# Kernel optimization log

Hardware: AMD Instinct MI355X
Metric: run time of the kernel (lower is better)

The kernel has to match this reference:

```python
import jax, jax.numpy as jnp
import numpy as np

B, T, C, H = 4, 4096, 1024, 64

def setup_inputs() -> dict:
    key = jax.random.key(0)
    k1, k2, k3, k4, k5 = jax.random.split(key, 5)
    scale = 0.02
    return {
        "x": jax.random.normal(k1, (B, T, C), dtype=jnp.float32),
        "head_bias": jax.random.normal(k2, (T, T), dtype=jnp.float32) * 0.1,
        "w_k": jax.random.normal(k3, (C, H), dtype=jnp.float32) * scale,
        "w_q": jax.random.normal(k4, (C, H), dtype=jnp.float32) * scale,
        "w_v": jax.random.normal(k5, (C, H), dtype=jnp.float32) * scale,
    }

def reference(x, head_bias, w_k, w_q, w_v):
    # x: (B,T,C) ; projections: (B,T,H)
    k = jnp.einsum('btc,ch->bth', x, w_k)
    q = jnp.einsum('btc,ch->bth', x, w_q)
    v = jnp.einsum('btc,ch->bth', x, w_v)
    Tq = x.shape[1]
    # scores: (B,T,T) with RPE bias and causal mask
    scores = jnp.einsum('bqh,bkh->bqk', q, k) * (k.shape[-1] ** -0.5)
    scores = scores + head_bias[None, :, :]
    causal = jnp.tril(jnp.ones((Tq, Tq), dtype=bool))
    scores = jnp.where(causal[None, :, :], scores, -jnp.inf)
    weights = jax.nn.softmax(scores, axis=-1)
    out = jnp.einsum('bqk,bkh->bqh', weights, v)
    return out
```

## Files before the change

kernel.cpp:

```cpp
#include <hip/hip_runtime.h>
#include <hip/hip_bf16.h>


#define T_DIM 4096
#define C_DIM 1024
#define CK    256

typedef __attribute__((ext_vector_type(8))) short s16x8;
typedef __attribute__((ext_vector_type(4))) float f32x4;
typedef __attribute__((ext_vector_type(2))) unsigned int u32x2;

__device__ __forceinline__ short f2bf(float f) {
    unsigned u = __builtin_bit_cast(unsigned, f);
    u += 0x7FFFu + ((u >> 16) & 1u);
    return (short)(u >> 16);
}
__device__ __forceinline__ unsigned pack2(float a, float b) {
    unsigned ua = __builtin_bit_cast(unsigned, a);
    unsigned ub = __builtin_bit_cast(unsigned, b);
    ua += 0x7FFFu + ((ua >> 16) & 1u);
    ub += 0x7FFFu + ((ub >> 16) & 1u);
    return __builtin_amdgcn_perm(ub, ua, 0x07060302u);
}
__device__ __forceinline__ float bf2f(short s) {
    unsigned u = ((unsigned)(unsigned short)s) << 16;
    return __builtin_bit_cast(float, u);
}
__device__ __forceinline__ int chunk_off(int qt) {
    int g = qt >> 4, r = qt & 15;
    return qt + 8 * g * (g - 1) + r * g;
}
__device__ __forceinline__ void async16(const short* g, short* l) {
    __builtin_amdgcn_global_load_lds(
        (const __attribute__((address_space(1))) unsigned int*)g,
        (__attribute__((address_space(3))) unsigned int*)l, 16, 0, 0);
}

__global__ __launch_bounds__(256) void prep_frag(
    const float* __restrict__ wk, const float* __restrict__ wq,
    const float* __restrict__ wv, short* __restrict__ wfrag)
{
    int ksAll = blockIdx.x, mat = blockIdx.y;
    const float* w = (mat == 0) ? wk : ((mat == 1) ? wq : wv);
    float sc = (mat == 1) ? 0.125f : 1.0f;
    int nt = threadIdx.x >> 6, lane = threadIdx.x & 63;
    int quad = lane >> 4, l15 = lane & 15;
    int h = nt * 16 + l15;
    int cb = ksAll * 32 + quad * 8;
    s16x8 v;
    #pragma unroll
    for (int j = 0; j < 8; ++j) v[j] = f2bf(w[(cb + j) * 64 + h] * sc);
    *(s16x8*)&wfrag[((ksAll * 12 + mat * 4 + nt) * 64 + lane) * 8] = v;
}

union ProjSmem {
    short xs[32][1032];
    struct {
        short comb[2][16][136];
        short vsep[64][40];
    } c;
};

__global__ __launch_bounds__(256, 2) void proj_fused(
    const float* __restrict__ x, const short* __restrict__ wfrag,
    short* __restrict__ qb, short* __restrict__ kfrag, short* __restrict__ vfrag)
{
    __shared__ __align__(16) ProjSmem sm;

    int tid = threadIdx.x;
    int w = tid >> 6, lane = tid & 63;
    int rt = w >> 1, h = w & 1;
    int l15 = lane & 15, quad = lane >> 4;
    int m0 = blockIdx.x * 32;

    s16x8 fA[12], fB[12];
    {
        const s16x8* fb = (const s16x8*)&wfrag[((size_t)(h * 16) * 12 * 64 + lane) * 8];
        #pragma unroll
        for (int f = 0; f < 12; ++f) fA[f] = fb[f * 64];
    }

    #pragma unroll 8
    for (int p = 0; p < 32; ++p) {
        f32x4 v = *(const f32x4*)&x[(size_t)(m0 + p) * C_DIM + tid * 4];
        u32x2 d;
        d[0] = pack2(v[0], v[1]);
        d[1] = pack2(v[2], v[3]);
        *(u32x2*)&sm.xs[p][tid * 4] = d;
    }
    __syncthreads();

    f32x4 acc[12];
    #pragma unroll
    for (int i = 0; i < 12; ++i) acc[i] = (f32x4){0.f, 0.f, 0.f, 0.f};

    #pragma unroll 1
    for (int ks = 0; ks < 16; ks += 2) {
        {
            const s16x8* fb = (const s16x8*)&wfrag[((size_t)(h * 16 + ks + 1) * 12 * 64 + lane) * 8];
            #pragma unroll
            for (int f = 0; f < 12; ++f) fB[f] = fb[f * 64];
        }
        s16x8 af = *(const s16x8*)&sm.xs[rt * 16 + l15][(h * 16 + ks) * 32 + quad * 8];
        #pragma unroll
        for (int f = 0; f < 12; ++f)
            acc[f] = __builtin_amdgcn_mfma_f32_16x16x32_bf16(af, fA[f], acc[f], 0, 0, 0);
        if (ks + 2 < 16) {
            const s16x8* fb = (const s16x8*)&wfrag[((size_t)(h * 16 + ks + 2) * 12 * 64 + lane) * 8];
            #pragma unroll
            for (int f = 0; f < 12; ++f) fA[f] = fb[f * 64];
        }
        s16x8 af2 = *(const s16x8*)&sm.xs[rt * 16 + l15][(h * 16 + ks + 1) * 32 + quad * 8];
        #pragma unroll
        for (int f = 0; f < 12; ++f)
            acc[f] = __builtin_amdgcn_mfma_f32_16x16x32_bf16(af2, fB[f], acc[f], 0, 0, 0);
    }
    __syncthreads();

    if (h == 1) {
        #pragma unroll
        for (int f = 0; f < 8; ++f)
            #pragma unroll
            for (int r = 0; r < 4; ++r)
                sm.c.comb[rt][quad * 4 + r][(f >> 2) * 64 + (f & 3) * 16 + l15] = f2bf(acc[f][r]);
        #pragma unroll
        for (int f = 8; f < 12; ++f)
            #pragma unroll
            for (int r = 0; r < 4; ++r)
                sm.c.vsep[(f & 3) * 16 + l15][rt * 16 + quad * 4 + r] = f2bf(acc[f][r]);
    }
    __syncthreads();
    if (h == 0) {
        #pragma unroll
        for (int f = 0; f < 8; ++f)
            #pragma unroll
            for (int r = 0; r < 4; ++r) {
                int col = (f >> 2) * 64 + (f & 3) * 16 + l15, rr = quad * 4 + r;
                sm.c.comb[rt][rr][col] = f2bf(acc[f][r] + bf2f(sm.c.comb[rt][rr][col]));
            }
        #pragma unroll
        for (int f = 8; f < 12; ++f)
            #pragma unroll
            for (int r = 0; r < 4; ++r) {
                int hh = (f & 3) * 16 + l15, kk = rt * 16 + quad * 4 + r;
                sm.c.vsep[hh][kk] = f2bf(acc[f][r] + bf2f(sm.c.vsep[hh][kk]));
            }
    }
    __syncthreads();

    int b = m0 >> 12, t0 = m0 & 4095;
    int t016 = t0 >> 4, kt32 = t0 >> 5;
    {
        int row = tid >> 3, ch = tid & 7;
        s16x8 v = *(const s16x8*)&sm.c.comb[row >> 4][row & 15][64 + ch * 8];
        *(s16x8*)&qb[(size_t)(m0 + row) * 64 + ch * 8] = v;
    }
    {
        int kt = w & 1, ks = w >> 1;
        s16x8 v = *(const s16x8*)&sm.c.comb[kt][l15][ks * 32 + quad * 8];
        *(s16x8*)&kfrag[(size_t)(((b * 256 + t016 + kt) * 2 + ks) * 64 + lane) * 8] = v;
    }
    {
        int nt = w;
        s16x8 v = *(const s16x8*)&sm.c.vsep[nt * 16 + l15][quad * 8];
        *(s16x8*)&vfrag[(size_t)(((b * 128 + kt32) * 4 + nt) * 64 + lane) * 8] = v;
    }
}

#define SOFT(N, AS, BV) do {                                                  \
    float _sv[4];                                                             \
    _Pragma("unroll")                                                         \
    for (int _r = 0; _r < 4; ++_r) {                                          \
        _sv[_r] = (AS)[_r] + (BV)[_r];                                        \
        if (mask_on && (kabs + (N) * 16 + quad * 4 + _r > q0 + l15))          \
            _sv[_r] = -__builtin_inff();                                      \
        float _p = __expf(_sv[_r]);                                           \
        _sv[_r] = _p;                                                         \
        l_sum += _p;                                                          \
    }                                                                         \
    u32x2 _d;                                                                 \
    _d[0] = pack2(_sv[0], _sv[1]);                                            \
    _d[1] = pack2(_sv[2], _sv[3]);                                            \
    *(u32x2*)&plds[w][l15][(N) * 16 + quad * 4] = _d;                         \
} while (0)

#define COMPUTEK(KREL, B0, B1) do {                                           \
    int _kt16 = (KREL) >> 4;                                                  \
    int _kt32 = (KREL) >> 5;                                                  \
    int kabs = kstart + (KREL);                                               \
    s16x8 _ak0 = *(const s16x8*)&klds[(_kt16 * 2 + 0) * 512 + lane * 8];      \
    s16x8 _ak1 = *(const s16x8*)&klds[(_kt16 * 2 + 1) * 512 + lane * 8];      \
    s16x8 _ak2 = *(const s16x8*)&klds[(_kt16 * 2 + 2) * 512 + lane * 8];      \
    s16x8 _ak3 = *(const s16x8*)&klds[(_kt16 * 2 + 3) * 512 + lane * 8];      \
    s16x8 _bv0 = *(const s16x8*)&vlds[(_kt32 * 4 + 0) * 512 + lane * 8];      \
    s16x8 _bv1 = *(const s16x8*)&vlds[(_kt32 * 4 + 1) * 512 + lane * 8];      \
    s16x8 _bv2 = *(const s16x8*)&vlds[(_kt32 * 4 + 2) * 512 + lane * 8];      \
    s16x8 _bv3 = *(const s16x8*)&vlds[(_kt32 * 4 + 3) * 512 + lane * 8];      \
    f32x4 _aS0 = (f32x4){0.f, 0.f, 0.f, 0.f};                                 \
    f32x4 _aS1 = (f32x4){0.f, 0.f, 0.f, 0.f};                                 \
    _aS0 = __builtin_amdgcn_mfma_f32_16x16x32_bf16(_ak0, aq0, _aS0, 0, 0, 0); \
    _aS0 = __builtin_amdgcn_mfma_f32_16x16x32_bf16(_ak1, aq1, _aS0, 0, 0, 0); \
    _aS1 = __builtin_amdgcn_mfma_f32_16x16x32_bf16(_ak2, aq0, _aS1, 0, 0, 0); \
    _aS1 = __builtin_amdgcn_mfma_f32_16x16x32_bf16(_ak3, aq1, _aS1, 0, 0, 0); \
    SOFT(0, _aS0, B0);                                                        \
    SOFT(1, _aS1, B1);                                                        \
    s16x8 _ap = *(const s16x8*)&plds[w][l15][quad * 8];                       \
    accO[0] = __builtin_amdgcn_mfma_f32_16x16x32_bf16(_ap, _bv0, accO[0], 0, 0, 0); \
    accO[1] = __builtin_amdgcn_mfma_f32_16x16x32_bf16(_ap, _bv1, accO[1], 0, 0, 0); \
    accO[2] = __builtin_amdgcn_mfma_f32_16x16x32_bf16(_ap, _bv2, accO[2], 0, 0, 0); \
    accO[3] = __builtin_amdgcn_mfma_f32_16x16x32_bf16(_ap, _bv3, accO[3], 0, 0, 0); \
} while (0)

__global__ __launch_bounds__(512, 4) void flash_part(
    const short* __restrict__ qb, const short* __restrict__ kfrag,
    const short* __restrict__ vfrag, const float* __restrict__ bias,
    short* __restrict__ po)
{
    int g = blockIdx.x;
    int c = blockIdx.y;
    int b = blockIdx.z;
    if (c > (g >> 1)) return;

    __shared__ __align__(16) short klds[32 * 512];
    __shared__ __align__(16) short vlds[32 * 512];
    __shared__ __align__(16) short plds[8][16][40];

    int tid = threadIdx.x;
    int w = tid >> 6, lane = tid & 63;
    int l15 = lane & 15, quad = lane >> 4;

    int qt = g * 8 + w;
    int q0 = qt * 16;
    int kstart = c * CK;
    int kend = min(kstart + CK, q0 + 16);
    int nk = kend - kstart;
    bool mask_on = (kend > q0);

    const short* ksrc = kfrag + (size_t)((b * 256 + c * 16) * 2) * 512;
    const short* vsrc = vfrag + (size_t)((b * 128 + c * 8) * 4) * 512;
    #pragma unroll
    for (int i = 0; i < 4; ++i) {
        int seg = i * 8 + w;
        async16(ksrc + (size_t)seg * 512 + lane * 8, &klds[seg * 512]);
    }
    #pragma unroll
    for (int i = 0; i < 4; ++i) {
        int seg = i * 8 + w;
        async16(vsrc + (size_t)seg * 512 + lane * 8, &vlds[seg * 512]);
    }

    const short* qrow = qb + (size_t)(b * T_DIM + q0 + l15) * 64;
    s16x8 aq0 = *(const s16x8*)(qrow + quad * 8);
    s16x8 aq1 = *(const s16x8*)(qrow + 32 + quad * 8);
    const float* brow = bias + (size_t)(q0 + l15) * T_DIM + kstart;
    f32x4 bA0 = *(const f32x4*)&brow[quad * 4];
    f32x4 bA1 = *(const f32x4*)&brow[16 + quad * 4];
    f32x4 bB0, bB1;

    float l_sum = 0.f;
    f32x4 accO[4];
    #pragma unroll
    for (int nt = 0; nt < 4; ++nt) accO[nt] = (f32x4){0.f, 0.f, 0.f, 0.f};

    __syncthreads();

    int krel = 0;
    while (true) {
        int kn = krel + 32;
        bool more = (kn < nk);
        if (more) {
            bB0 = *(const f32x4*)&brow[kn + quad * 4];
            bB1 = *(const f32x4*)&brow[kn + 16 + quad * 4];
        }
        COMPUTEK(krel, bA0, bA1);
        if (!more) break;
        krel = kn; kn = krel + 32;
        bool more2 = (kn < nk);
        if (more2) {
            bA0 = *(const f32x4*)&brow[kn + quad * 4];
            bA1 = *(const f32x4*)&brow[kn + 16 + quad * 4];
        }
        COMPUTEK(krel, bB0, bB1);
        if (!more2) break;
        krel = kn;
    }

    l_sum += __shfl_xor(l_sum, 16, 64);
    l_sum += __shfl_xor(l_sum, 32, 64);

    short* base = po + (size_t)((chunk_off(qt) + c) * 4 + b) * 1040;
    #pragma unroll
    for (int nt = 0; nt < 4; ++nt)
        #pragma unroll
        for (int r = 0; r < 4; ++r)
            base[(quad * 4 + r) * 64 + nt * 16 + l15] = f2bf(accO[nt][r]);
    if (quad == 0) base[1024 + l15] = f2bf(l_sum);
}

__global__ __launch_bounds__(256) void flash_reduce(
    const short* __restrict__ po, float* __restrict__ out)
{
    int idx = blockIdx.x * 256 + threadIdx.x;
    int row = idx >> 3, c8 = idx & 7;
    int b = row >> 12, t = row & 4095;
    int qt = t >> 4, rloc = t & 15;
    int nc = (t >> 8) + 1;
    int off = chunk_off(qt);
    float o[8];
    #pragma unroll
    for (int j = 0; j < 8; ++j) o[j] = 0.f;
    float l = 0.f;
    #pragma unroll 1
    for (int cc = 0; cc < nc; ++cc) {
        const short* base = po + (size_t)((off + cc) * 4 + b) * 1040;
        s16x8 v = *(const s16x8*)&base[rloc * 64 + c8 * 8];
        #pragma unroll
        for (int j = 0; j < 8; ++j) o[j] += bf2f(v[j]);
        l += bf2f(base[1024 + rloc]);
    }
    float inv = 1.0f / l;
    f32x4 r0 = (f32x4){o[0] * inv, o[1] * inv, o[2] * inv, o[3] * inv};
    f32x4 r1 = (f32x4){o[4] * inv, o[5] * inv, o[6] * inv, o[7] * inv};
    float* op = &out[(size_t)row * 64 + c8 * 8];
    *(f32x4*)op = r0;
    *(f32x4*)(op + 4) = r1;
}

extern "C" void kernel_launch(void* const* d_in, const int* in_sizes, int n_in,
                              void* d_out, int out_size, void* d_ws, size_t ws_size,
                              hipStream_t stream) {
    (void)in_sizes; (void)n_in; (void)out_size; (void)ws_size;
    const float* x    = (const float*)d_in[0];
    const float* bias = (const float*)d_in[1];
    const float* wk   = (const float*)d_in[2];
    const float* wq   = (const float*)d_in[3];
    const float* wv   = (const float*)d_in[4];
    float* out = (float*)d_out;

    short* wfrag = (short*)d_ws;
    short* qb    = wfrag + 196608;
    short* kfrag = qb + 1048576;
    short* vfrag = kfrag + 1048576;
    short* po    = vfrag + 1048576;

    prep_frag<<<dim3(32, 3), dim3(256), 0, stream>>>(wk, wq, wv, wfrag);
    proj_fused<<<dim3(512), dim3(256), 0, stream>>>(x, wfrag, qb, kfrag, vfrag);
    flash_part<<<dim3(32, 16, 4), dim3(512), 0, stream>>>(qb, kfrag, vfrag, bias, po);
    flash_reduce<<<dim3(512), dim3(256), 0, stream>>>(po, out);
}
```

Baseline: 204.5 us.

## Double-buffer K/V staging in 64-key slices and shuffle P via permlane swaps

Replaces the single upfront load of the full 256-key K/V chunk into LDS with double-buffered 64-key slices, so the async copy of the next slice overlaps compute on the current one. Bias prefetch moves to 64-key granularity. The probability tile no longer round-trips through LDS; it is rearranged into MFMA A-operand layout with v_permlane32/16_swap instructions. LDS drops substantially and the occupancy hint rises from 4 to 6, at the cost of a __syncthreads per slice and extra register pressure.

After: 234.3 us. +14.6%, slower.

```diff
diff --git a/kernel.cpp b/kernel.cpp
--- a/kernel.cpp
+++ b/kernel.cpp
@@ -5,10 +5,12 @@
 #define T_DIM 4096
 #define C_DIM 1024
 #define CK    256
+#define SK    64
 
 typedef __attribute__((ext_vector_type(8))) short s16x8;
 typedef __attribute__((ext_vector_type(4))) float f32x4;
 typedef __attribute__((ext_vector_type(2))) unsigned int u32x2;
+typedef __attribute__((ext_vector_type(4))) unsigned int u32x4;
 
 __device__ __forceinline__ short f2bf(float f) {
     unsigned u = __builtin_bit_cast(unsigned, f);
@@ -167,7 +169,19 @@
     }
 }
 
-#define SOFT(N, AS, BV) do {                                                  \
+#define STAGE(S, KB, VB) do {                                                 \
+    async16(ksrc + (size_t)((S) * 8 + w) * 512 + lane * 8, &KB[w * 512]);     \
+    async16(vsrc + (size_t)((S) * 8 + w) * 512 + lane * 8, &VB[w * 512]);     \
+} while (0)
+
+#define BIAS4(KREL, D0, D1, D2, D3) do {                                      \
+    D0 = *(const f32x4*)&brow[(KREL) + quad * 4];                             \
+    D1 = *(const f32x4*)&brow[(KREL) + 16 + quad * 4];                        \
+    D2 = *(const f32x4*)&brow[(KREL) + 32 + quad * 4];                        \
+    D3 = *(const f32x4*)&brow[(KREL) + 48 + quad * 4];                        \
+} while (0)
+
+#define SOFT(N, AS, BV, PLO, PHI) do {                                        \
     float _sv[4];                                                             \
     _Pragma("unroll")                                                         \
     for (int _r = 0; _r < 4; ++_r) {                                          \
@@ -178,40 +192,44 @@
         _sv[_r] = _p;                                                         \
         l_sum += _p;                                                          \
     }                                                                         \
-    u32x2 _d;                                                                 \
-    _d[0] = pack2(_sv[0], _sv[1]);                                            \
-    _d[1] = pack2(_sv[2], _sv[3]);                                            \
-    *(u32x2*)&plds[w][l15][(N) * 16 + quad * 4] = _d;                         \
+    PLO = pack2(_sv[0], _sv[1]);                                              \
+    PHI = pack2(_sv[2], _sv[3]);                                              \
 } while (0)
 
-#define COMPUTEK(KREL, B0, B1) do {                                           \
-    int _kt16 = (KREL) >> 4;                                                  \
-    int _kt32 = (KREL) >> 5;                                                  \
+#define COMPUTEK(KB, VB, KREL, B0, B1) do {                                   \
+    int _lt = (((KREL) & 63) >> 4);                               \
+    int _lv = (((KREL) & 63) >> 5);                               \
     int kabs = kstart + (KREL);                                               \
-    s16x8 _ak0 = *(const s16x8*)&klds[(_kt16 * 2 + 0) * 512 + lane * 8];      \
-    s16x8 _ak1 = *(const s16x8*)&klds[(_kt16 * 2 + 1) * 512 + lane * 8];      \
-    s16x8 _ak2 = *(const s16x8*)&klds[(_kt16 * 2 + 2) * 512 + lane * 8];      \
-    s16x8 _ak3 = *(const s16x8*)&klds[(_kt16 * 2 + 3) * 512 + lane * 8];      \
-    s16x8 _bv0 = *(const s16x8*)&vlds[(_kt32 * 4 + 0) * 512 + lane * 8];      \
-    s16x8 _bv1 = *(const s16x8*)&vlds[(_kt32 * 4 + 1) * 512 + lane * 8];      \
-    s16x8 _bv2 = *(const s16x8*)&vlds[(_kt32 * 4 + 2) * 512 + lane * 8];      \
-    s16x8 _bv3 = *(const s16x8*)&vlds[(_kt32 * 4 + 3) * 512 + lane * 8];      \
+    s16x8 _ak0 = *(const s16x8*)&KB[(_lt * 2 + 0) * 512 + lane * 8];          \
+    s16x8 _ak1 = *(const s16x8*)&KB[(_lt * 2 + 1) * 512 + lane * 8];          \
+    s16x8 _ak2 = *(const s16x8*)&KB[(_lt * 2 + 2) * 512 + lane * 8];          \
+    s16x8 _ak3 = *(const s16x8*)&KB[(_lt * 2 + 3) * 512 + lane * 8];          \
     f32x4 _aS0 = (f32x4){0.f, 0.f, 0.f, 0.f};                                 \
     f32x4 _aS1 = (f32x4){0.f, 0.f, 0.f, 0.f};                                 \
     _aS0 = __builtin_amdgcn_mfma_f32_16x16x32_bf16(_ak0, aq0, _aS0, 0, 0, 0); \
     _aS0 = __builtin_amdgcn_mfma_f32_16x16x32_bf16(_ak1, aq1, _aS0, 0, 0, 0); \
     _aS1 = __builtin_amdgcn_mfma_f32_16x16x32_bf16(_ak2, aq0, _aS1, 0, 0, 0); \
     _aS1 = __builtin_amdgcn_mfma_f32_16x16x32_bf16(_ak3, aq1, _aS1, 0, 0, 0); \
-    SOFT(0, _aS0, B0);                                                        \
-    SOFT(1, _aS1, B1);                                                        \
-    s16x8 _ap = *(const s16x8*)&plds[w][l15][quad * 8];                       \
+    unsigned _p0, _p1, _p2, _p3;                                              \
+    SOFT(0, _aS0, B0, _p0, _p1);                                              \
+    SOFT(1, _aS1, B1, _p2, _p3);                                              \
+    asm("v_permlane32_swap_b32 %0, %1" : "+v"(_p0), "+v"(_p2));               \
+    asm("v_permlane16_swap_b32 %0, %1" : "+v"(_p0), "+v"(_p2));               \
+    asm("v_permlane32_swap_b32 %0, %1" : "+v"(_p1), "+v"(_p3));               \
+    asm("v_permlane16_swap_b32 %0, %1" : "+v"(_p1), "+v"(_p3));               \
+    u32x4 _apu = (u32x4){_p0, _p1, _p2, _p3};                                 \
+    s16x8 _ap = __builtin_bit_cast(s16x8, _apu);                              \
+    s16x8 _bv0 = *(const s16x8*)&VB[(_lv * 4 + 0) * 512 + lane * 8];          \
+    s16x8 _bv1 = *(const s16x8*)&VB[(_lv * 4 + 1) * 512 + lane * 8];          \
+    s16x8 _bv2 = *(const s16x8*)&VB[(_lv * 4 + 2) * 512 + lane * 8];          \
+    s16x8 _bv3 = *(const s16x8*)&VB[(_lv * 4 + 3) * 512 + lane * 8];          \
     accO[0] = __builtin_amdgcn_mfma_f32_16x16x32_bf16(_ap, _bv0, accO[0], 0, 0, 0); \
     accO[1] = __builtin_amdgcn_mfma_f32_16x16x32_bf16(_ap, _bv1, accO[1], 0, 0, 0); \
     accO[2] = __builtin_amdgcn_mfma_f32_16x16x32_bf16(_ap, _bv2, accO[2], 0, 0, 0); \
     accO[3] = __builtin_amdgcn_mfma_f32_16x16x32_bf16(_ap, _bv3, accO[3], 0, 0, 0); \
 } while (0)
 
-__global__ __launch_bounds__(512, 4) void flash_part(
+__global__ __launch_bounds__(512, 6) void flash_part(
     const short* __restrict__ qb, const short* __restrict__ kfrag,
     const short* __restrict__ vfrag, const float* __restrict__ bias,
     short* __restrict__ po)
@@ -221,9 +239,10 @@
     int b = blockIdx.z;
     if (c > (g >> 1)) return;
 
-    __shared__ __align__(16) short klds[32 * 512];
-    __shared__ __align__(16) short vlds[32 * 512];
-    __shared__ __align__(16) short plds[8][16][40];
+    __shared__ __align__(16) short klds0[8 * 512];
+    __shared__ __align__(16) short klds1[8 * 512];
+    __shared__ __align__(16) short vlds0[8 * 512];
+    __shared__ __align__(16) short vlds1[8 * 512];
 
     int tid = threadIdx.x;
     int w = tid >> 6, lane = tid & 63;
@@ -234,28 +253,20 @@
     int kstart = c * CK;
     int kend = min(kstart + CK, q0 + 16);
     int nk = kend - kstart;
+    int nkb = min(CK, 128 * g + 128 - kstart);
+    int nsub = (nkb + SK - 1) / SK;
     bool mask_on = (kend > q0);
 
     const short* ksrc = kfrag + (size_t)((b * 256 + c * 16) * 2) * 512;
     const short* vsrc = vfrag + (size_t)((b * 128 + c * 8) * 4) * 512;
-    #pragma unroll
-    for (int i = 0; i < 4; ++i) {
-        int seg = i * 8 + w;
-        async16(ksrc + (size_t)seg * 512 + lane * 8, &klds[seg * 512]);
-    }
-    #pragma unroll
-    for (int i = 0; i < 4; ++i) {
-        int seg = i * 8 + w;
-        async16(vsrc + (size_t)seg * 512 + lane * 8, &vlds[seg * 512]);
-    }
-
+
+    STAGE(0, klds0, vlds0);
     const short* qrow = qb + (size_t)(b * T_DIM + q0 + l15) * 64;
     s16x8 aq0 = *(const s16x8*)(qrow + quad * 8);
     s16x8 aq1 = *(const s16x8*)(qrow + 32 + quad * 8);
     const float* brow = bias + (size_t)(q0 + l15) * T_DIM + kstart;
-    f32x4 bA0 = *(const f32x4*)&brow[quad * 4];
-    f32x4 bA1 = *(const f32x4*)&brow[16 + quad * 4];
-    f32x4 bB0, bB1;
+    f32x4 bA0, bA1, bA2, bA3, bB0, bB1, bB2, bB3;
+    BIAS4(0, bA0, bA1, bA2, bA3);
 
     float l_sum = 0.f;
     f32x4 accO[4];
@@ -264,25 +275,24 @@
 
     __syncthreads();
 
-    int krel = 0;
+    int s = 0, krel = 0;
     while (true) {
-        int kn = krel + 32;
-        bool more = (kn < nk);
-        if (more) {
-            bB0 = *(const f32x4*)&brow[kn + quad * 4];
-            bB1 = *(const f32x4*)&brow[kn + 16 + quad * 4];
-        }
-        COMPUTEK(krel, bA0, bA1);
-        if (!more) break;
-        krel = kn; kn = krel + 32;
-        bool more2 = (kn < nk);
-        if (more2) {
-            bA0 = *(const f32x4*)&brow[kn + quad * 4];
-            bA1 = *(const f32x4*)&brow[kn + 16 + quad * 4];
-        }
-        COMPUTEK(krel, bB0, bB1);
-        if (!more2) break;
-        krel = kn;
+        bool hn = (s + 1 < nsub);
+        if (hn) STAGE(s + 1, klds1, vlds1);
+        if (krel < nk)      COMPUTEK(klds0, vlds0, krel, bA0, bA1);
+        if (krel + 32 < nk) COMPUTEK(klds0, vlds0, krel + 32, bA2, bA3);
+        if (hn) BIAS4(krel + 64, bB0, bB1, bB2, bB3);
+        __syncthreads();
+        if (!hn) break;
+        ++s; krel += SK;
+        bool hn2 = (s + 1 < nsub);
+        if (hn2) STAGE(s + 1, klds0, vlds0);
+        if (krel < nk)      COMPUTEK(klds1, vlds1, krel, bB0, bB1);
+        if (krel + 32 < nk) COMPUTEK(klds1, vlds1, krel + 32, bB2, bB3);
+        if (hn2) BIAS4(krel + 64, bA0, bA1, bA2, bA3);
+        __syncthreads();
+        if (!hn2) break;
+        ++s; krel += SK;
     }
 
     l_sum += __shfl_xor(l_sum, 16, 64);
```
